# Kernel optimization log

Measured on AMD Instinct MI355X. Metric: run time of the kernel, lower is better.

## Reference

```python
import jax, jax.numpy as jnp
import numpy as np

VOXEL = 64        # voxel_size from init_kwargs
SHARPNESS = 100.0 # sigmoid sharpness in original forward
EPS = 1e-8


def make_coords(V):
    # Grid of (x, y) points in [0,1]^2, row-major over (y, x) like torch.meshgrid 'ij'.
    y, x = jnp.meshgrid(jnp.arange(V), jnp.arange(V), indexing='ij')
    coords = jnp.stack([x.ravel(), y.ravel()], axis=1).astype(jnp.float32)
    return coords / np.float32(V - 1)  # [M, 2], M = V*V


def setup_inputs() -> dict:
    key = jax.random.key(0)
    k1, k2, k3 = jax.random.split(key, 3)
    B, N, P = 8, 32, 32
    # Vertices uniform in [0,1)^2: all rows sum != 0, so the original's per-vertex
    # validity mask keeps every vertex (P >= 3), matching this static-shape reference.
    polygons = jax.random.uniform(k1, (B, N, P, 2), dtype=jnp.float32)
    attributes = jax.random.uniform(k2, (B, 4), dtype=jnp.float32)
    validity_scores = jax.random.uniform(k3, (B, N), dtype=jnp.float32)
    return {"polygons": polygons, "attributes": attributes, "validity_scores": validity_scores}


def _polygon_sdf(polygons, coords):
    # polygons: [B, N, P, 2]; coords: [M, 2] -> sdf [B, N, M]
    v0 = polygons[:, :, :, None, :]                         # [B,N,P,1,2]
    v1 = jnp.roll(polygons, shift=-1, axis=2)[:, :, :, None, :]
    pts = coords[None, None, None, :, :]                    # [1,1,1,M,2]
    e = v1 - v0                                             # edge vectors
    v = pts - v0                                            # point - vertex
    e_norm_sq = (e * e).sum(-1, keepdims=True) + EPS
    t = jnp.clip((v * e).sum(-1, keepdims=True) / e_norm_sq, 0.0, 1.0)
    diff = v - t * e                                        # pts - projection
    dists = jnp.sqrt((diff * diff).sum(-1))                 # [B,N,P,M]
    min_dist = dists.min(axis=2)                            # [B,N,M]

    # Crossing-number inside test
    x_pts = coords[None, None, None, :, 0]                  # [1,1,1,M]
    y_pts = coords[None, None, None, :, 1]
    x0, y0 = v0[..., 0], v0[..., 1]                         # [B,N,P,1]
    x1, y1 = v1[..., 0], v1[..., 1]
    y_crosses = ((y0 <= y_pts) & (y1 > y_pts)) | ((y1 <= y_pts) & (y0 > y_pts))
    inter_x = x0 + (x1 - x0) * ((y_pts - y0) / (y1 - y0 + EPS))
    crossings = (inter_x > x_pts) & y_crosses               # [B,N,P,M]
    inside = (crossings.sum(axis=2) % 2) == 1               # [B,N,M]
    return jnp.where(inside, -min_dist, min_dist)


def reference(polygons, attributes, validity_scores):
    B, N, P, _ = polygons.shape
    V = VOXEL
    coords = make_coords(V)                                 # [M,2]
    sdf = _polygon_sdf(polygons, coords)                    # [B,N,M]

    valid = validity_scores >= 0.5                          # [B,N]
    sdf = jnp.where(valid[:, :, None], sdf, 1.0)            # invalid polys -> sdf = 1
    masks = jax.nn.sigmoid(-sdf * SHARPNESS)                # [B,N,M]
    # Combined max only over valid polygons (invalid contribute 0, like the zero-init max loop)
    combined = jnp.where(valid[:, :, None], masks, 0.0).max(axis=1)  # [B,M]
    combined = combined.reshape(B, V, V)                    # [B,H,W]

    # height_voxels = clamp(int(attr0 * D), 1, D)
    h = jnp.clip(jnp.floor(attributes[:, 0] * V).astype(jnp.int32), 1, V)  # [B]
    depth_mask = (jnp.arange(V)[None, :] < h[:, None]).astype(combined.dtype)  # [B,D]
    voxels = depth_mask[:, :, None, None] * combined[:, None, :, :]  # [B,D,H,W]
    return voxels
```

## Files before the change

### kernel.cpp

```cpp
#include <hip/hip_runtime.h>
#include <math.h>

#define VOX 64
#define NPOLY 32
#define NEDGE 32
#define NEDGES_TOT (NPOLY * NEDGE)
#define GROUPS 4
#define POLY_PER_GROUP (NPOLY / GROUPS)

__global__ __launch_bounds__(256, 2) void extrusion_kernel(
    const float* __restrict__ polygons,
    const float* __restrict__ attributes,
    const float* __restrict__ validity,
    float* __restrict__ out)
{
    __shared__ float4 eA[NEDGES_TOT];
    __shared__ float4 eB[NEDGES_TOT];
    __shared__ float  partial[GROUPS][VOX];
    __shared__ float  comb[VOX];
    __shared__ int    validF[NPOLY];

    const int t   = threadIdx.x;
    const int b   = blockIdx.x >> 6;
    const int row = blockIdx.x & 63;
    const float py = (float)row * (1.0f / 63.0f);
    const float px = (float)(t & 63) * (1.0f / 63.0f);

    if (t < NPOLY) validF[t] = (validity[b * NPOLY + t] >= 0.5f) ? 1 : 0;

    const float2* pb = (const float2*)(polygons + (size_t)b * NPOLY * NEDGE * 2);
    for (int e = t; e < NEDGES_TOT; e += 256) {
        int n  = e >> 5;
        int k  = e & 31;
        int k1 = (k + 1) & 31;
        float2 v0 = pb[n * NEDGE + k];
        float2 v1 = pb[n * NEDGE + k1];
        float ex = v1.x - v0.x;
        float ey = v1.y - v0.y;
        float inv   = 1.0f / (ex * ex + ey * ey + 1e-8f);
        float slope = ex / (ey + 1e-8f);
        eA[e] = make_float4(v0.x, v0.y, ex, ey);
        eB[e] = make_float4(inv, slope, v1.y, 0.0f);
    }
    __syncthreads();

    const int g = t >> 6;
    float minsdf = 1e30f;
    for (int nn = 0; nn < POLY_PER_GROUP; ++nn) {
        int n = g * POLY_PER_GROUP + nn;
        if (!validF[n]) continue;
        float mind2  = 1e30f;
        int   parity = 0;
        int   base   = n * NEDGE;
        #pragma unroll 4
        for (int k = 0; k < NEDGE; ++k) {
            float4 A  = eA[base + k];
            float4 Bv = eB[base + k];
            float vx = px - A.x;
            float vy = py - A.y;
            float dot = vx * A.z + vy * A.w;
            float tt  = fminf(fmaxf(dot * Bv.x, 0.0f), 1.0f);
            float dx = vx - tt * A.z;
            float dy = vy - tt * A.w;
            float d2 = dx * dx + dy * dy;
            mind2 = fminf(mind2, d2);
            bool a  = (A.y  <= py);
            bool bb = (Bv.z <= py);
            float ix = fmaf(Bv.y, vy, A.x);
            parity ^= ((a != bb) && (ix > px)) ? 1 : 0;
        }
        float d   = sqrtf(mind2);
        float sdf = parity ? -d : d;
        minsdf = fminf(minsdf, sdf);
    }
    partial[g][t & 63] = minsdf;
    __syncthreads();

    if (t < VOX) {
        float m = fminf(fminf(partial[0][t], partial[1][t]),
                        fminf(partial[2][t], partial[3][t]));
        comb[t] = 1.0f / (1.0f + __expf(100.0f * m));
    }
    __syncthreads();

    float att = attributes[b * 4 + 0];
    int h = (int)floorf(att * 64.0f);
    h = max(1, min(64, h));

    float4* out4 = (float4*)out;
    const int q  = t & 15;
    const int zs = t >> 4;
    float4 cv = make_float4(comb[q * 4 + 0], comb[q * 4 + 1],
                            comb[q * 4 + 2], comb[q * 4 + 3]);
    float4 zero = make_float4(0.f, 0.f, 0.f, 0.f);
    size_t base4 = (size_t)b * 65536 + (size_t)row * 16 + q;
    #pragma unroll
    for (int it = 0; it < 4; ++it) {
        int z = it * 16 + zs;
        out4[base4 + (size_t)z * 1024] = (z < h) ? cv : zero;
    }
}

extern "C" void kernel_launch(void* const* d_in, const int* in_sizes, int n_in,
                              void* d_out, int out_size, void* d_ws, size_t ws_size,
                              hipStream_t stream) {
    const float* polygons   = (const float*)d_in[0];
    const float* attributes = (const float*)d_in[1];
    const float* validity   = (const float*)d_in[2];
    float* out = (float*)d_out;
    const int B = in_sizes[2] / NPOLY;
    dim3 grid(B * VOX);
    dim3 block(256);
    extrusion_kernel<<<grid, block, 0, stream>>>(polygons, attributes, validity, out);
}
```

Baseline: 76.06 us.

## Compact valid polygons, precompute row-specific crossings, and double block size

Valid polygon indices are compacted with a wavefront ballot so the eight thread groups share the valid polygons evenly, with no divergent skip branches. Because each block handles a single row, the per-edge y-dependent terms (the y offset, its product with the edge y component, and the crossing x-intercept or a sentinel) are computed once in shared memory, which shrinks the inner loop to a few FMAs and one compare. The block grows to 512 threads, giving 8 polygon groups and 2 output stores per thread. In exchange the prologue does more work per edge, and the larger block may limit occupancy.

```diff
diff --git a/kernel.cpp b/kernel.cpp
--- a/kernel.cpp
+++ b/kernel.cpp
@@ -4,32 +4,35 @@
 #define VOX 64
 #define NPOLY 32
 #define NEDGE 32
-#define NEDGES_TOT (NPOLY * NEDGE)
-#define GROUPS 4
-#define POLY_PER_GROUP (NPOLY / GROUPS)
+#define NET (NPOLY * NEDGE)
 
-__global__ __launch_bounds__(256, 2) void extrusion_kernel(
+__global__ __launch_bounds__(512, 2) void extrusion_kernel(
     const float* __restrict__ polygons,
     const float* __restrict__ attributes,
     const float* __restrict__ validity,
     float* __restrict__ out)
 {
-    __shared__ float4 eA[NEDGES_TOT];
-    __shared__ float4 eB[NEDGES_TOT];
-    __shared__ float  partial[GROUPS][VOX];
+    __shared__ float4 ecA[NET];
+    __shared__ float4 ecB[NET];
+    __shared__ float  partial[8][VOX];
     __shared__ float  comb[VOX];
-    __shared__ int    validF[NPOLY];
+    __shared__ int    vIdx[NPOLY];
+    __shared__ int    nValidS;
 
     const int t   = threadIdx.x;
     const int b   = blockIdx.x >> 6;
     const int row = blockIdx.x & 63;
     const float py = (float)row * (1.0f / 63.0f);
-    const float px = (float)(t & 63) * (1.0f / 63.0f);
 
-    if (t < NPOLY) validF[t] = (validity[b * NPOLY + t] >= 0.5f) ? 1 : 0;
+    if (t < 64) {
+        bool f = (t < NPOLY) && (validity[b * NPOLY + t] >= 0.5f);
+        unsigned long long m = __ballot(f);
+        if (f) vIdx[__popcll(m & ((1ull << t) - 1ull))] = t;
+        if (t == 0) nValidS = (int)__popcll(m);
+    }
 
-    const float2* pb = (const float2*)(polygons + (size_t)b * NPOLY * NEDGE * 2);
-    for (int e = t; e < NEDGES_TOT; e += 256) {
+    const float2* pb = (const float2*)(polygons + (size_t)b * NET * 2);
+    for (int e = t; e < NET; e += 512) {
         int n  = e >> 5;
         int k  = e & 31;
         int k1 = (k + 1) & 31;
@@ -37,68 +40,64 @@
         float2 v1 = pb[n * NEDGE + k1];
         float ex = v1.x - v0.x;
         float ey = v1.y - v0.y;
-        float inv   = 1.0f / (ex * ex + ey * ey + 1e-8f);
-        float slope = ex / (ey + 1e-8f);
-        eA[e] = make_float4(v0.x, v0.y, ex, ey);
-        eB[e] = make_float4(inv, slope, v1.y, 0.0f);
+        float inv = 1.0f / (ex * ex + ey * ey + 1e-8f);
+        float vy  = py - v0.y;
+        float c1  = vy * ey;
+        bool ycross = ((v0.y <= py) && (v1.y > py)) || ((v1.y <= py) && (v0.y > py));
+        float ix = ycross ? (v0.x + ex * (vy / (ey + 1e-8f))) : -1e30f;
+        ecA[e] = make_float4(v0.x, ex, ey, inv);
+        ecB[e] = make_float4(c1, vy, ix, 0.0f);
     }
     __syncthreads();
 
-    const int g = t >> 6;
+    const int g  = t >> 6;
+    const int lx = t & 63;
+    const float px = (float)lx * (1.0f / 63.0f);
+    const int nV = nValidS;
     float minsdf = 1e30f;
-    for (int nn = 0; nn < POLY_PER_GROUP; ++nn) {
-        int n = g * POLY_PER_GROUP + nn;
-        if (!validF[n]) continue;
-        float mind2  = 1e30f;
-        int   parity = 0;
-        int   base   = n * NEDGE;
-        #pragma unroll 4
+    for (int j = g; j < nV; j += 8) {
+        int base = vIdx[j] * NEDGE;
+        float mind2 = 1e30f;
+        int cnt = 0;
+        #pragma unroll
         for (int k = 0; k < NEDGE; ++k) {
-            float4 A  = eA[base + k];
-            float4 Bv = eB[base + k];
-            float vx = px - A.x;
-            float vy = py - A.y;
-            float dot = vx * A.z + vy * A.w;
-            float tt  = fminf(fmaxf(dot * Bv.x, 0.0f), 1.0f);
-            float dx = vx - tt * A.z;
-            float dy = vy - tt * A.w;
-            float d2 = dx * dx + dy * dy;
+            float4 A  = ecA[base + k];
+            float4 Bc = ecB[base + k];
+            float vx  = px - A.x;
+            float dot = fmaf(vx, A.y, Bc.x);
+            float tt  = fminf(fmaxf(dot * A.w, 0.0f), 1.0f);
+            float dx  = fmaf(-tt, A.y, vx);
+            float dy  = fmaf(-tt, A.z, Bc.y);
+            float d2  = fmaf(dy, dy, dx * dx);
             mind2 = fminf(mind2, d2);
-            bool a  = (A.y  <= py);
-            bool bb = (Bv.z <= py);
-            float ix = fmaf(Bv.y, vy, A.x);
-            parity ^= ((a != bb) && (ix > px)) ? 1 : 0;
+            cnt += (Bc.z > px) ? 1 : 0;
         }
-        float d   = sqrtf(mind2);
-        float sdf = parity ? -d : d;
-        minsdf = fminf(minsdf, sdf);
+        float d = sqrtf(mind2);
+        minsdf = fminf(minsdf, (cnt & 1) ? -d : d);
     }
-    partial[g][t & 63] = minsdf;
+    partial[g][lx] = minsdf;
     __syncthreads();
 
     if (t < VOX) {
-        float m = fminf(fminf(partial[0][t], partial[1][t]),
-                        fminf(partial[2][t], partial[3][t]));
+        float m = partial[0][t];
+        #pragma unroll
+        for (int gg = 1; gg < 8; ++gg) m = fminf(m, partial[gg][t]);
         comb[t] = 1.0f / (1.0f + __expf(100.0f * m));
     }
     __syncthreads();
 
     float att = attributes[b * 4 + 0];
-    int h = (int)floorf(att * 64.0f);
-    h = max(1, min(64, h));
+    int h = max(1, min(64, (int)floorf(att * 64.0f)));
 
     float4* out4 = (float4*)out;
     const int q  = t & 15;
-    const int zs = t >> 4;
+    const int z0 = t >> 4;
     float4 cv = make_float4(comb[q * 4 + 0], comb[q * 4 + 1],
                             comb[q * 4 + 2], comb[q * 4 + 3]);
     float4 zero = make_float4(0.f, 0.f, 0.f, 0.f);
     size_t base4 = (size_t)b * 65536 + (size_t)row * 16 + q;
-    #pragma unroll
-    for (int it = 0; it < 4; ++it) {
-        int z = it * 16 + zs;
-        out4[base4 + (size_t)z * 1024] = (z < h) ? cv : zero;
-    }
+    out4[base4 + (size_t)z0 * 1024]        = (z0 < h)        ? cv : zero;
+    out4[base4 + (size_t)(z0 + 32) * 1024] = ((z0 + 32) < h) ? cv : zero;
 }
 
 extern "C" void kernel_launch(void* const* d_in, const int* in_sizes, int n_in,
@@ -110,6 +109,6 @@
     float* out = (float*)d_out;
     const int B = in_sizes[2] / NPOLY;
     dim3 grid(B * VOX);
-    dim3 block(256);
+    dim3 block(512);
     extrusion_kernel<<<grid, block, 0, stream>>>(polygons, attributes, validity, out);
 }
```

Measured after the change: 70.51 us. 7.3% less time.
